# Optimization experiments

Hardware: AMD Instinct MI355X
Metric: run time of the kernel (lower is better)

Reference implementation:

```python
import jax, jax.numpy as jnp
import numpy as np

EPS = 1e-5

def _layernorm(x, gamma):
    # LayerNorm over last dim, no bias (torch LayerNorm(bias=False))
    mu = jnp.mean(x, axis=-1, keepdims=True)
    var = jnp.mean(jnp.square(x - mu), axis=-1, keepdims=True)
    return (x - mu) * jax.lax.rsqrt(var + EPS) * gamma

def setup_inputs() -> dict:
    B, N, D = 32, 1024, 512
    key = jax.random.key(0)
    ks = jax.random.split(key, 6)
    x = jax.random.normal(ks[0], (B, N, D), dtype=jnp.float32)
    # valid lengths in [1, N] so no query row has all keys masked
    belief_base_sizes = jax.random.randint(ks[1], (B,), 1, N + 1, dtype=jnp.int32)
    s = 0.02
    w_qkv = jax.random.normal(ks[2], (D, 3 * D), dtype=jnp.float32) * s
    w_fc = jax.random.normal(ks[3], (D, D), dtype=jnp.float32) * s
    w_proj = jax.random.normal(ks[4], (D, D), dtype=jnp.float32) * s
    g1 = jnp.ones((D,), dtype=jnp.float32)
    g2 = jnp.ones((D,), dtype=jnp.float32)
    return {"x": x, "belief_base_sizes": belief_base_sizes, "g1": g1,
            "w_qkv": w_qkv, "g2": g2, "w_fc": w_fc, "w_proj": w_proj}

def reference(x, belief_base_sizes, g1, w_qkv, g2, w_fc, w_proj):
    B, N, D = x.shape
    h = _layernorm(x, g1)                      # LN1
    qkv = jnp.einsum('bnd,de->bne', h, w_qkv)  # [B,N,3D]
    q, k, v = jnp.split(qkv, 3, axis=-1)
    scores = jnp.einsum('bqd,bkd->bqk', q, k) / jnp.sqrt(jnp.float32(D))
    # mask key columns >= valid size (rows are NOT masked, matching the original)
    col = jnp.arange(N)
    pad = col[None, None, :] >= belief_base_sizes[:, None, None]  # [B,1,N]
    scores = jnp.where(pad, -jnp.inf, scores)
    attn = jax.nn.softmax(scores, axis=-1)
    y = jnp.einsum('bqk,bkd->bqd', attn, v)
    y = _layernorm(y, g2)                      # LN2 (no residual in original)
    y = jnp.einsum('bnd,de->bne', y, w_fc)
    y = jax.nn.gelu(y, approximate=False)      # torch GELU default = exact erf
    y = jnp.einsum('bnd,de->bne', y, w_proj)
    return y
```

## Files before the change

kernel.cpp:

```cpp
#include <hip/hip_runtime.h>
#include <hip/hip_bf16.h>
#include <cmath>


using f16 = _Float16;
typedef _Float16 f16x8 __attribute__((ext_vector_type(8)));
typedef _Float16 f16x4 __attribute__((ext_vector_type(4)));
typedef _Float16 f16x2 __attribute__((ext_vector_type(2)));
typedef float f32x4 __attribute__((ext_vector_type(4)));

#define NB 32
#define NN 1024
#define ND 512

#define GLOAD_LDS16(g, l)                                                     \
    __builtin_amdgcn_global_load_lds(                                         \
        (const __attribute__((address_space(1))) void*)(g),                   \
        (__attribute__((address_space(3))) void*)(l), 16, 0, 0)

__global__ void transpose_cast_all(const float* __restrict__ wqkv, f16* __restrict__ wqkvT,
                                   const float* __restrict__ wfc, f16* __restrict__ wfcT,
                                   const float* __restrict__ wproj, f16* __restrict__ wprojT) {
    const int z = blockIdx.z;
    const float* w = (z == 0) ? wqkv : (z == 1) ? wfc : wproj;
    f16* wT       = (z == 0) ? wqkvT : (z == 1) ? wfcT : wprojT;
    const int Ncols = (z == 0) ? 1536 : 512;
    if ((int)blockIdx.x * 32 >= Ncols) return;

    __shared__ float tile[32][33];
    const int n0 = blockIdx.x * 32, k0 = blockIdx.y * 32;
    const int tx = threadIdx.x, ty = threadIdx.y;
    for (int i = ty; i < 32; i += 8)
        tile[i][tx] = w[(long long)(k0 + i) * Ncols + n0 + tx];
    __syncthreads();
    for (int i = ty; i < 32; i += 8)
        wT[(long long)(n0 + i) * 512 + k0 + tx] = (f16)tile[tx][i];
}

template <typename TIN>
__global__ __launch_bounds__(256) void ln_kernel(const TIN* __restrict__ x,
                                                 const float* __restrict__ gamma,
                                                 f16* __restrict__ out) {
    const int tid = threadIdx.x;
    const long long base = (long long)blockIdx.x * ND;
    float v0, v1;
    if constexpr (sizeof(TIN) == 4) {
        const float2 t = ((const float2*)(x + base))[tid];
        v0 = t.x; v1 = t.y;
    } else {
        const f16x2 t = ((const f16x2*)(x + base))[tid];
        v0 = (float)t.x; v1 = (float)t.y;
    }

    __shared__ float red[8];
    const int wave = tid >> 6, lane = tid & 63;

    float s = v0 + v1;
#pragma unroll
    for (int o = 32; o > 0; o >>= 1) s += __shfl_down(s, o, 64);
    if (lane == 0) red[wave] = s;
    __syncthreads();
    const float mean = (red[0] + red[1] + red[2] + red[3]) * (1.f / 512.f);
    __syncthreads();

    const float d0 = v0 - mean, d1 = v1 - mean;
    float q = d0 * d0 + d1 * d1;
#pragma unroll
    for (int o = 32; o > 0; o >>= 1) q += __shfl_down(q, o, 64);
    if (lane == 0) red[wave] = q;
    __syncthreads();
    const float var = (red[0] + red[1] + red[2] + red[3]) * (1.f / 512.f);
    const float rstd = rsqrtf(var + 1e-5f);

    f16x2 o2;
    o2.x = (f16)(d0 * rstd * gamma[2 * tid]);
    o2.y = (f16)(d1 * rstd * gamma[2 * tid + 1]);
    ((f16x2*)(out + base))[tid] = o2;
}

__global__ __launch_bounds__(256) void softmax_wave(f16* __restrict__ scores,
                                                    const int* __restrict__ sizes) {
    const int b = blockIdx.y;
    const int wave = threadIdx.x >> 6, lane = threadIdx.x & 63;
    const int row = blockIdx.x * 4 + wave;
    f16* srow = scores + ((long long)b * NN + row) * NN;
    const int sz = sizes[b];
    const int keff = (sz + 63) & ~63;
    const int cbase = lane * 16;

    float v[16];
    if (cbase < keff) {
        const f16x8 a0 = *(const f16x8*)&srow[cbase];
        const f16x8 a1 = *(const f16x8*)&srow[cbase + 8];
#pragma unroll
        for (int e = 0; e < 8; e++) { v[e] = (float)a0[e]; v[8 + e] = (float)a1[e]; }
    } else {
#pragma unroll
        for (int e = 0; e < 16; e++) v[e] = 0.f;
    }

    float m = -1e30f;
#pragma unroll
    for (int e = 0; e < 16; e++)
        if (cbase + e < sz) m = fmaxf(m, v[e]);
#pragma unroll
    for (int o = 32; o > 0; o >>= 1) m = fmaxf(m, __shfl_xor(m, o, 64));

    float s = 0.f;
#pragma unroll
    for (int e = 0; e < 16; e++) {
        v[e] = (cbase + e < sz) ? __expf(v[e] - m) : 0.f;
        s += v[e];
    }
#pragma unroll
    for (int o = 32; o > 0; o >>= 1) s += __shfl_xor(s, o, 64);
    const float inv = 1.f / s;

    if (cbase < keff) {
        f16x8 o0, o1;
#pragma unroll
        for (int e = 0; e < 8; e++) {
            o0[e] = (f16)(v[e] * inv);
            o1[e] = (f16)(v[8 + e] * inv);
        }
        *(f16x8*)&srow[cbase] = o0;
        *(f16x8*)&srow[cbase + 8] = o1;
    }
}

__device__ __forceinline__ float gelu_exact(float x) {
    return 0.5f * x * (1.f + erff(x * 0.70710678118654752f));
}

template <int MODE, int MASKN, int MASKK>
__global__ __launch_bounds__(256) void gemm_bt(
    const f16* __restrict__ A, int lda, long long strideA,
    const f16* __restrict__ Bt, int ldb, long long strideB,
    void* __restrict__ Cv, int ldc, long long strideC,
    int K, float alpha, const int* __restrict__ sizes, void* __restrict__ Cv2) {
    __shared__ __align__(16) f16 As[128 * 64];
    __shared__ __align__(16) f16 Bs[128 * 64];

    const int tid = threadIdx.x;
    const int wave = tid >> 6, lane = tid & 63;
    const int wr = (wave >> 1) * 64, wc = (wave & 1) * 64;
    const int lrow = lane & 15, quad = lane >> 4;

    int bx = blockIdx.x, by = blockIdx.y;
    if (gridDim.z == 1) {
        const int gx = gridDim.x;
        const int nwg = gx * (int)gridDim.y;
        const int id = by * gx + bx;
        const int q = nwg >> 3, r = nwg & 7;
        const int xcd = id & 7, slot = id >> 3;
        const int wid = (xcd < r) ? (xcd * (q + 1) + slot)
                                  : (r * (q + 1) + (xcd - r) * q + slot);
        bx = wid % gx;
        by = wid / gx;
    }
    const long long m0 = (long long)by * 128;
    const long long n0 = (long long)bx * 128;

    if (MASKN) {
        if (n0 >= sizes[blockIdx.z]) return;
    }
    int Keff = K;
    if (MASKK) {
        const int ke = (sizes[blockIdx.z] + 63) & ~63;
        if (ke < Keff) Keff = ke;
    }

    A += (long long)blockIdx.z * strideA;
    Bt += (long long)blockIdx.z * strideB;

    f32x4 acc[4][4];
#pragma unroll
    for (int i = 0; i < 4; i++)
#pragma unroll
        for (int j = 0; j < 4; j++) acc[i][j] = (f32x4){0.f, 0.f, 0.f, 0.f};

    const f16* Ap[4];
    const f16* Bp[4];
#pragma unroll
    for (int p = 0; p < 4; p++) {
        const int s = tid + p * 256;
        const int r = s >> 3, c = ((s & 7) ^ (r & 7)) * 8;
        Ap[p] = A + (m0 + r) * lda + c;
        Bp[p] = Bt + (n0 + r) * ldb + c;
    }

    for (int k0 = 0; k0 < Keff; k0 += 64) {
        __syncthreads();
#pragma unroll
        for (int p = 0; p < 4; p++) GLOAD_LDS16(Ap[p] + k0, &As[(tid + p * 256) * 8]);
#pragma unroll
        for (int p = 0; p < 4; p++) GLOAD_LDS16(Bp[p] + k0, &Bs[(tid + p * 256) * 8]);
        __syncthreads();

#pragma unroll
        for (int h = 0; h < 2; h++) {
            const int gq = ((h * 4 + quad) ^ (lrow & 7)) * 8;
            f16x8 af[4], bf[4];
#pragma unroll
            for (int i = 0; i < 4; i++)
                af[i] = *(const f16x8*)&As[(wr + i * 16 + lrow) * 64 + gq];
#pragma unroll
            for (int j = 0; j < 4; j++)
                bf[j] = *(const f16x8*)&Bs[(wc + j * 16 + lrow) * 64 + gq];
#pragma unroll
            for (int i = 0; i < 4; i++)
#pragma unroll
                for (int j = 0; j < 4; j++)
                    acc[i][j] = __builtin_amdgcn_mfma_f32_16x16x32_f16(af[i], bf[j], acc[i][j], 0, 0, 0);
        }
    }

    if (MODE == 3 && n0 >= 1024) {
        f16* vTp = (f16*)Cv2;
#pragma unroll
        for (int i = 0; i < 4; i++) {
            const long long rbase = m0 + wr + i * 16 + quad * 4;
            const long long bb = rbase >> 10;
            const long long nrow = rbase & 1023;
#pragma unroll
            for (int j = 0; j < 4; j++) {
                const long long col = n0 + wc + j * 16 + lrow - 1024;
                f16x4 pk;
#pragma unroll
                for (int r = 0; r < 4; r++) pk[r] = (f16)acc[i][j][r];
                *(f16x4*)&vTp[bb * ND * NN + col * NN + nrow] = pk;
            }
        }
        return;
    }
    float* Cf = (float*)Cv + (long long)blockIdx.z * strideC;
    f16* Ch = (f16*)Cv + (long long)blockIdx.z * strideC;
#pragma unroll
    for (int i = 0; i < 4; i++) {
        const long long rbase = m0 + wr + i * 16 + quad * 4;
#pragma unroll
        for (int j = 0; j < 4; j++) {
            const long long col = n0 + wc + j * 16 + lrow;
#pragma unroll
            for (int r = 0; r < 4; r++) {
                float vv = acc[i][j][r];
                if (MODE == 1) {
                    Cf[(rbase + r) * ldc + col] = vv * alpha;
                } else if (MODE == 2) {
                    Ch[(rbase + r) * ldc + col] = (f16)gelu_exact(vv);
                } else {
                    Ch[(rbase + r) * ldc + col] = (f16)(vv * alpha);
                }
            }
        }
    }
}

extern "C" void kernel_launch(void* const* d_in, const int* in_sizes, int n_in,
                              void* d_out, int out_size, void* d_ws, size_t ws_size,
                              hipStream_t stream) {
    const float* x     = (const float*)d_in[0];
    const int*   sizes = (const int*)d_in[1];
    const float* g1    = (const float*)d_in[2];
    const float* wqkv  = (const float*)d_in[3];
    const float* g2    = (const float*)d_in[4];
    const float* wfc   = (const float*)d_in[5];
    const float* wproj = (const float*)d_in[6];
    float* out = (float*)d_out;
    char* ws = (char*)d_ws;

    f16* wqkvT  = (f16*)(ws + (0ull << 20));
    f16* wfcT   = (f16*)(ws + (2ull << 20));
    f16* wprojT = (f16*)(ws + (3ull << 20));
    f16* qk     = (f16*)(ws + (4ull << 20));
    f16* vT     = (f16*)(ws + (68ull << 20));
    f16* y      = (f16*)(ws + (4ull << 20));
    f16* ln2o   = (f16*)(ws + (36ull << 20));
    f16* gelub  = (f16*)(ws + (68ull << 20));

    f16* h      = (f16*)d_out;
    f16* scores = (f16*)d_out;

    const long long sstr = (long long)NN * NN;
    const long long qstr = (long long)NN * 1024;
    const long long vstr = (long long)ND * NN;
    const long long ystr = (long long)NN * ND;

    transpose_cast_all<<<dim3(48, 16, 3), dim3(32, 8), 0, stream>>>(
        wqkv, wqkvT, wfc, wfcT, wproj, wprojT);

    ln_kernel<float><<<NB * NN, 256, 0, stream>>>(x, g1, h);

    gemm_bt<3, 0, 0><<<dim3(12, 256, 1), 256, 0, stream>>>(
        h, 512, 0, wqkvT, 512, 0, qk, 1024, 0, 512, 1.0f, nullptr, vT);

    gemm_bt<0, 1, 0><<<dim3(8, 8, 32), 256, 0, stream>>>(
        qk, 1024, qstr, qk + 512, 1024, qstr,
        scores, NN, sstr, 512, 0.044194173824159216f, sizes, nullptr);

    softmax_wave<<<dim3(NN / 4, NB), 256, 0, stream>>>(scores, sizes);

    gemm_bt<0, 0, 1><<<dim3(4, 8, 32), 256, 0, stream>>>(
        scores, NN, sstr, vT, NN, vstr,
        y, ND, ystr, NN, 1.0f, sizes, nullptr);

    ln_kernel<f16><<<NB * NN, 256, 0, stream>>>(y, g2, ln2o);

    gemm_bt<2, 0, 0><<<dim3(4, 256, 1), 256, 0, stream>>>(
        ln2o, 512, 0, wfcT, 512, 0, gelub, 512, 0, 512, 1.0f, nullptr, nullptr);

    gemm_bt<1, 0, 0><<<dim3(4, 256, 1), 256, 0, stream>>>(
        gelub, 512, 0, wprojT, 512, 0, out, 512, 0, 512, 1.0f, nullptr, nullptr);
}
```

Measured before the change: 409.0 us.

## Add 256x256-tile GEMM with 4-stage LDS pipeline for dense projections

Adds a new gemm256 kernel using 256x256 output tiles, 512 threads and a 4-deep global_load_lds ring buffer with a K-step of 32, explicit vmcnt waits and MFMA priority raising. The QKV, FC+GELU and output projection GEMMs now use it in place of the 128x128 gemm_bt, which is reduced to the batched attention paths only. The aim is more data reuse per tile and better overlap of loads with MFMA. The cost is 128KB of dynamic LDS and a small grid for the N=512 GEMMs (256 workgroups), which may leave CUs underused. The K loop is hardcoded to 16 steps, so it only works for K=512.

```diff
diff --git a/kernel.cpp b/kernel.cpp
--- a/kernel.cpp
+++ b/kernel.cpp
@@ -132,6 +132,147 @@
     return 0.5f * x * (1.f + erff(x * 0.70710678118654752f));
 }
 
+#define STAGE256(t)                                                           \
+    { f16* sl = lds + ((t) & 3) * 16384;                                      \
+      GLOAD_LDS16(Ap[0] + (t) * 32, sl + tid * 8);                            \
+      GLOAD_LDS16(Ap[1] + (t) * 32, sl + (tid + 512) * 8);                    \
+      GLOAD_LDS16(Bp[0] + (t) * 32, sl + 8192 + tid * 8);                     \
+      GLOAD_LDS16(Bp[1] + (t) * 32, sl + 8192 + (tid + 512) * 8); }
+
+#define COMPUTE256(t)                                                         \
+    { const f16* As_ = lds + ((t) & 3) * 16384;                               \
+      const f16* Bs_ = As_ + 8192;                                            \
+      f16x8 af[8], bf[4];                                                     \
+      _Pragma("unroll") for (int i = 0; i < 8; i++)                           \
+          af[i] = *(const f16x8*)&As_[(wr + i * 16 + lrow) * 32 + gq];        \
+      _Pragma("unroll") for (int j = 0; j < 4; j++)                           \
+          bf[j] = *(const f16x8*)&Bs_[(wc + j * 16 + lrow) * 32 + gq];        \
+      __builtin_amdgcn_s_setprio(1);                                          \
+      _Pragma("unroll") for (int i = 0; i < 8; i++)                           \
+      _Pragma("unroll") for (int j = 0; j < 4; j++)                           \
+          acc[i][j] = __builtin_amdgcn_mfma_f32_16x16x32_f16(af[i], bf[j], acc[i][j], 0, 0, 0); \
+      __builtin_amdgcn_s_setprio(0); }
+
+#define SYNC256(n)                                                            \
+    __builtin_amdgcn_sched_barrier(0);                                        \
+    asm volatile("s_waitcnt vmcnt(" #n ")" ::: "memory");                     \
+    __builtin_amdgcn_s_barrier();                                             \
+    asm volatile("" ::: "memory");
+
+template <int MODE>
+__global__ __launch_bounds__(512, 2) void gemm256(
+    const f16* __restrict__ A, int lda,
+    const f16* __restrict__ Bt, int ldb,
+    void* __restrict__ Cv, int ldc, void* __restrict__ Cv2) {
+    extern __shared__ __align__(16) f16 lds[];
+
+    const int tid = threadIdx.x;
+    const int wave = tid >> 6, lane = tid & 63;
+    const int wr = (wave >> 2) * 128, wc = (wave & 3) * 64;
+    const int lrow = lane & 15, quad = lane >> 4;
+    const int gq = (quad ^ ((lrow >> 1) & 3)) * 8;
+
+    const int gx = gridDim.x;
+    const int nwg = gx * (int)gridDim.y;
+    const int id = blockIdx.y * gx + blockIdx.x;
+    const int wid = (id & 7) * (nwg >> 3) + (id >> 3);
+    const int m0 = (wid / gx) * 256;
+    const int n0 = (wid % gx) * 256;
+
+    f32x4 acc[8][4];
+#pragma unroll
+    for (int i = 0; i < 8; i++)
+#pragma unroll
+        for (int j = 0; j < 4; j++) acc[i][j] = (f32x4){0.f, 0.f, 0.f, 0.f};
+
+    const f16* Ap[2];
+    const f16* Bp[2];
+#pragma unroll
+    for (int p = 0; p < 2; p++) {
+        const int s = tid + p * 512;
+        const int r = s >> 2, g = s & 3;
+        const int c = (g ^ ((r >> 1) & 3)) * 8;
+        Ap[p] = A + (long long)(m0 + r) * lda + c;
+        Bp[p] = Bt + (long long)(n0 + r) * ldb + c;
+    }
+
+    STAGE256(0); STAGE256(1); STAGE256(2);
+
+    for (int t = 0; t < 13; ++t) {
+        SYNC256(8);
+        STAGE256(t + 3);
+        COMPUTE256(t);
+    }
+    SYNC256(8);
+    COMPUTE256(13);
+    SYNC256(4);
+    COMPUTE256(14);
+    SYNC256(0);
+    COMPUTE256(15);
+
+    const int cbase = n0 + wc + lrow;
+    if constexpr (MODE == 3) {
+        if (n0 >= 1024) {
+            f16* vTp = (f16*)Cv2;
+#pragma unroll
+            for (int i = 0; i < 8; i++) {
+                const int rbase = m0 + wr + i * 16 + quad * 4;
+                const int bb = rbase >> 10, nrow = rbase & 1023;
+                f16* vb = vTp + (long long)bb * (ND * NN) + nrow;
+#pragma unroll
+                for (int j = 0; j < 4; j++) {
+                    const int col = cbase + j * 16 - 1024;
+                    f16x4 pk;
+#pragma unroll
+                    for (int r = 0; r < 4; r++) pk[r] = (f16)acc[i][j][r];
+                    *(f16x4*)&vb[(long long)col * NN] = pk;
+                }
+            }
+            return;
+        }
+        f16* Ch = (f16*)Cv;
+#pragma unroll
+        for (int i = 0; i < 8; i++) {
+            const int rbase = m0 + wr + i * 16 + quad * 4;
+#pragma unroll
+            for (int j = 0; j < 4; j++) {
+                const int col = cbase + j * 16;
+#pragma unroll
+                for (int r = 0; r < 4; r++)
+                    Ch[(long long)(rbase + r) * ldc + col] = (f16)acc[i][j][r];
+            }
+        }
+        return;
+    }
+    if constexpr (MODE == 1) {
+        float* Cf = (float*)Cv;
+#pragma unroll
+        for (int i = 0; i < 8; i++) {
+            const int rbase = m0 + wr + i * 16 + quad * 4;
+#pragma unroll
+            for (int j = 0; j < 4; j++) {
+                const int col = cbase + j * 16;
+#pragma unroll
+                for (int r = 0; r < 4; r++)
+                    Cf[(long long)(rbase + r) * ldc + col] = acc[i][j][r];
+            }
+        }
+    } else {
+        f16* Ch = (f16*)Cv;
+#pragma unroll
+        for (int i = 0; i < 8; i++) {
+            const int rbase = m0 + wr + i * 16 + quad * 4;
+#pragma unroll
+            for (int j = 0; j < 4; j++) {
+                const int col = cbase + j * 16;
+#pragma unroll
+                for (int r = 0; r < 4; r++)
+                    Ch[(long long)(rbase + r) * ldc + col] = (f16)gelu_exact(acc[i][j][r]);
+            }
+        }
+    }
+}
+
 template <int MODE, int MASKN, int MASKK>
 __global__ __launch_bounds__(256) void gemm_bt(
     const f16* __restrict__ A, int lda, long long strideA,
@@ -145,21 +286,8 @@
     const int wave = tid >> 6, lane = tid & 63;
     const int wr = (wave >> 1) * 64, wc = (wave & 1) * 64;
     const int lrow = lane & 15, quad = lane >> 4;
-
-    int bx = blockIdx.x, by = blockIdx.y;
-    if (gridDim.z == 1) {
-        const int gx = gridDim.x;
-        const int nwg = gx * (int)gridDim.y;
-        const int id = by * gx + bx;
-        const int q = nwg >> 3, r = nwg & 7;
-        const int xcd = id & 7, slot = id >> 3;
-        const int wid = (xcd < r) ? (xcd * (q + 1) + slot)
-                                  : (r * (q + 1) + (xcd - r) * q + slot);
-        bx = wid % gx;
-        by = wid / gx;
-    }
-    const long long m0 = (long long)by * 128;
-    const long long n0 = (long long)bx * 128;
+    const long long m0 = (long long)blockIdx.y * 128;
+    const long long n0 = (long long)blockIdx.x * 128;
 
     if (MASKN) {
         if (n0 >= sizes[blockIdx.z]) return;
@@ -215,25 +343,6 @@
         }
     }
 
-    if (MODE == 3 && n0 >= 1024) {
-        f16* vTp = (f16*)Cv2;
-#pragma unroll
-        for (int i = 0; i < 4; i++) {
-            const long long rbase = m0 + wr + i * 16 + quad * 4;
-            const long long bb = rbase >> 10;
-            const long long nrow = rbase & 1023;
-#pragma unroll
-            for (int j = 0; j < 4; j++) {
-                const long long col = n0 + wc + j * 16 + lrow - 1024;
-                f16x4 pk;
-#pragma unroll
-                for (int r = 0; r < 4; r++) pk[r] = (f16)acc[i][j][r];
-                *(f16x4*)&vTp[bb * ND * NN + col * NN + nrow] = pk;
-            }
-        }
-        return;
-    }
-    float* Cf = (float*)Cv + (long long)blockIdx.z * strideC;
     f16* Ch = (f16*)Cv + (long long)blockIdx.z * strideC;
 #pragma unroll
     for (int i = 0; i < 4; i++) {
@@ -242,16 +351,8 @@
         for (int j = 0; j < 4; j++) {
             const long long col = n0 + wc + j * 16 + lrow;
 #pragma unroll
-            for (int r = 0; r < 4; r++) {
-                float vv = acc[i][j][r];
-                if (MODE == 1) {
-                    Cf[(rbase + r) * ldc + col] = vv * alpha;
-                } else if (MODE == 2) {
-                    Ch[(rbase + r) * ldc + col] = (f16)gelu_exact(vv);
-                } else {
-                    Ch[(rbase + r) * ldc + col] = (f16)(vv * alpha);
-                }
-            }
+            for (int r = 0; r < 4; r++)
+                Ch[(rbase + r) * ldc + col] = (f16)(acc[i][j][r] * alpha);
         }
     }
 }
@@ -286,13 +387,15 @@
     const long long vstr = (long long)ND * NN;
     const long long ystr = (long long)NN * ND;
 
+    const size_t LDSB = 131072;
+
     transpose_cast_all<<<dim3(48, 16, 3), dim3(32, 8), 0, stream>>>(
         wqkv, wqkvT, wfc, wfcT, wproj, wprojT);
 
     ln_kernel<float><<<NB * NN, 256, 0, stream>>>(x, g1, h);
 
-    gemm_bt<3, 0, 0><<<dim3(12, 256, 1), 256, 0, stream>>>(
-        h, 512, 0, wqkvT, 512, 0, qk, 1024, 0, 512, 1.0f, nullptr, vT);
+    gemm256<3><<<dim3(6, 128), 512, LDSB, stream>>>(
+        h, 512, wqkvT, 512, qk, 1024, vT);
 
     gemm_bt<0, 1, 0><<<dim3(8, 8, 32), 256, 0, stream>>>(
         qk, 1024, qstr, qk + 512, 1024, qstr,
@@ -306,9 +409,9 @@
 
     ln_kernel<f16><<<NB * NN, 256, 0, stream>>>(y, g2, ln2o);
 
-    gemm_bt<2, 0, 0><<<dim3(4, 256, 1), 256, 0, stream>>>(
-        ln2o, 512, 0, wfcT, 512, 0, gelub, 512, 0, 512, 1.0f, nullptr, nullptr);
-
-    gemm_bt<1, 0, 0><<<dim3(4, 256, 1), 256, 0, stream>>>(
-        gelub, 512, 0, wprojT, 512, 0, out, 512, 0, 512, 1.0f, nullptr, nullptr);
-}
+    gemm256<2><<<dim3(2, 128), 512, LDSB, stream>>>(
+        ln2o, 512, wfcT, 512, gelub, 512, nullptr);
+
+    gemm256<1><<<dim3(2, 128), 512, LDSB, stream>>>(
+        gelub, 512, wprojT, 512, out, 512, nullptr);
+}
```

Measured after the change: 392.3 us. -4.1%, faster.
